# Kernel tuning notes

Hardware: AMD Instinct MI355X
Metric: run time of the kernel (lower is better)

The kernel has to match this reference:

```python
import jax, jax.numpy as jnp
import numpy as np

N = 50000
E = 800000
F_IN = 256
HID = 96
N_CLS = 32
NEG_SLOPE = 0.2


def setup_inputs() -> dict:
    key = jax.random.key(0)
    ks = jax.random.split(key, 10)
    x = jax.random.normal(ks[0], (N, F_IN), dtype=jnp.float32)
    edge_index = jax.random.randint(ks[1], (2, E), 0, N, dtype=jnp.int64)
    s1 = 1.0 / np.sqrt(F_IN)
    s2 = 1.0 / np.sqrt(HID)
    return {
        "x": x,
        "edge_index": edge_index,
        "W1": jax.random.normal(ks[2], (F_IN, HID), dtype=jnp.float32) * s1,
        "a1_src": jax.random.normal(ks[3], (HID,), dtype=jnp.float32) * s2,
        "a1_dst": jax.random.normal(ks[4], (HID,), dtype=jnp.float32) * s2,
        "b1": jnp.zeros((HID,), dtype=jnp.float32),
        "W2": jax.random.normal(ks[5], (HID, N_CLS), dtype=jnp.float32) * s2,
        "a2_src": jax.random.normal(ks[6], (N_CLS,), dtype=jnp.float32) * (1.0 / np.sqrt(N_CLS)),
        "a2_dst": jax.random.normal(ks[7], (N_CLS,), dtype=jnp.float32) * (1.0 / np.sqrt(N_CLS)),
        "b2": jnp.zeros((N_CLS,), dtype=jnp.float32),
    }


def _gat_conv(x, src, dst, W, a_src, a_dst, b, n_nodes):
    # single-head GATConv (PyG defaults), self-loops already in src/dst
    h = x @ W                                  # [N, out]
    alpha_src = h @ a_src                      # [N]
    alpha_dst = h @ a_dst                      # [N]
    e = alpha_src[src] + alpha_dst[dst]        # [E'] edge logits (msg j->i: dst groups)
    e = jnp.where(e > 0, e, NEG_SLOPE * e)     # leaky_relu
    # segment softmax over edges grouped by destination node
    m = jax.ops.segment_max(e, dst, num_segments=n_nodes)
    ex = jnp.exp(e - m[dst])
    denom = jax.ops.segment_sum(ex, dst, num_segments=n_nodes)
    alpha = ex / denom[dst]                    # [E']
    out = jax.ops.segment_sum(alpha[:, None] * h[src], dst, num_segments=n_nodes)
    return out + b


def reference(x, edge_index, W1, a1_src, a1_dst, b1, W2, a2_src, a2_dst, b2):
    loops = jnp.arange(N, dtype=edge_index.dtype)
    src = jnp.concatenate([edge_index[0], loops])
    dst = jnp.concatenate([edge_index[1], loops])
    h = _gat_conv(x, src, dst, W1, a1_src, a1_dst, b1, N)
    h = jax.nn.elu(h)
    # dropout omitted (eval mode, training=False)
    out = _gat_conv(h, src, dst, W2, a2_src, a2_dst, b2, N)
    return jax.nn.log_softmax(out, axis=1)
```

## Files before the change

kernel.cpp:

```cpp
#include <hip/hip_runtime.h>
#include <cstdint>
#include <cstddef>

#define NNODES 50000
#define NEDGES 800000
#define MEDGES (NEDGES + NNODES)
#define FIN    256
#define HID    96
#define NCLS   32
#define NEG_SLOPE 0.2f

#define NBUCK  391
#define BCAP   3072

typedef unsigned int uint32;
typedef __attribute__((ext_vector_type(8))) short short8;
typedef __attribute__((ext_vector_type(4))) float f32x4;

__device__ __forceinline__ ushort bf_round(float f) {
    uint32 u = __float_as_uint(f);
    u += 0x7FFFu + ((u >> 16) & 1u);
    return (ushort)(u >> 16);
}
__device__ __forceinline__ uint32 pack_bf16x2(float a, float b) {
    return (uint32)bf_round(a) | ((uint32)bf_round(b) << 16);
}
__device__ __forceinline__ float bf_lo(uint32 u) { return __uint_as_float(u << 16); }
__device__ __forceinline__ float bf_hi(uint32 u) { return __uint_as_float(u & 0xFFFF0000u); }
__device__ __forceinline__ float lrelu(float t) { return (t > 0.f) ? t : NEG_SLOPE * t; }
__device__ __forceinline__ float af(int i) { return __int_as_float(i); }


__global__ __launch_bounds__(256) void bucket1_kernel(const int* __restrict__ ei,
                                                      int* __restrict__ gcount,
                                                      int* __restrict__ staging) {
    __shared__ int hist[NBUCK];
    __shared__ int base_sh[NBUCK];
    for (int i = threadIdx.x; i < NBUCK; i += 256) hist[i] = 0;
    __syncthreads();

    int v[8], rk[8], bk[8];
    int e0 = blockIdx.x * 2048;
#pragma unroll
    for (int i = 0; i < 8; ++i) {
        int e = e0 + i * 256 + threadIdx.x;
        if (e < MEDGES) {
            int s, d;
            if (e < NEDGES) { s = ei[e]; d = ei[NEDGES + e]; }
            else            { s = e - NEDGES; d = s; }
            bk[i] = d >> 7;
            v[i]  = s | ((d & 127) << 16);
            rk[i] = atomicAdd(&hist[bk[i]], 1);
        } else bk[i] = -1;
    }
    __syncthreads();
    for (int i = threadIdx.x; i < NBUCK; i += 256) {
        int c = hist[i];
        base_sh[i] = c ? atomicAdd(&gcount[i], c) : 0;
    }
    __syncthreads();
#pragma unroll
    for (int i = 0; i < 8; ++i) {
        if (bk[i] >= 0) {
            int pos = base_sh[bk[i]] + rk[i];
            if (pos < BCAP)
                staging[(size_t)bk[i] * BCAP + pos] = v[i];
        }
    }
}

__global__ __launch_bounds__(512) void bscan_kernel(const int* __restrict__ gcount,
                                                    int* __restrict__ bbase) {
    __shared__ int sd[512];
    int t = threadIdx.x;
    int v = (t < NBUCK) ? gcount[t] : 0;
    sd[t] = v;
    __syncthreads();
    for (int off = 1; off < 512; off <<= 1) {
        int val = (t >= off) ? sd[t - off] : 0;
        __syncthreads();
        sd[t] += val;
        __syncthreads();
    }
    if (t < NBUCK) bbase[t] = sd[t] - v;
}

__global__ __launch_bounds__(256) void bucket2_kernel(const int* __restrict__ staging,
                                                      const int* __restrict__ gcount,
                                                      const int* __restrict__ bbase,
                                                      int* __restrict__ rowptr,
                                                      int* __restrict__ esrc) {
    __shared__ int dcount[128];
    __shared__ int dincl[128];
    __shared__ int dexcl[128];
    __shared__ int fillc[128];

    const int b     = blockIdx.x;
    const int t     = threadIdx.x;
    const int cnt   = gcount[b];
    const int ebase = bbase[b];
    const int node0 = b << 7;
    const int* st   = staging + (size_t)b * BCAP;

    for (int i = t; i < 128; i += 256) { dcount[i] = 0; fillc[i] = 0; }
    __syncthreads();

    for (int i = t; i < cnt; i += 256)
        atomicAdd(&dcount[st[i] >> 16], 1);
    __syncthreads();

    if (t < 128) dincl[t] = dcount[t];
    __syncthreads();
    for (int off = 1; off < 128; off <<= 1) {
        int val = (t >= off && t < 128) ? dincl[t - off] : 0;
        __syncthreads();
        if (t < 128) dincl[t] += val;
        __syncthreads();
    }
    if (t < 128) {
        int excl = dincl[t] - dcount[t];
        dexcl[t] = excl;
        int node = node0 + t;
        if (node < NNODES) rowptr[node] = ebase + excl;
    }
    if (b == NBUCK - 1 && t == 0) rowptr[NNODES] = MEDGES;
    __syncthreads();

    for (int i = t; i < cnt; i += 256) {
        int v = st[i];
        int dd = v >> 16;
        int r = atomicAdd(&fillc[dd], 1);
        esrc[ebase + dexcl[dd] + r] = v & 0xFFFF;
    }
}


__global__ __launch_bounds__(256) void packw_kernel(const float* __restrict__ W1,
                                                    const float* __restrict__ W2,
                                                    ushort* __restrict__ W1p,
                                                    ushort* __restrict__ W2p) {
    for (int idx = threadIdx.x; idx < 6 * 8 * 64 * 8; idx += 256) {
        int j     = idx & 7;
        int lane  = (idx >> 3) & 63;
        int kstep = (idx >> 9) & 7;
        int ntile = idx >> 12;
        int k = kstep * 32 + ((lane >> 4) << 3) + j;
        int n = ntile * 16 + (lane & 15);
        W1p[idx] = bf_round(W1[(size_t)k * 96 + n]);
    }
    for (int idx = threadIdx.x; idx < 2 * 3 * 64 * 8; idx += 256) {
        int j     = idx & 7;
        int lane  = (idx >> 3) & 63;
        int kstep = (idx >> 9) % 3;
        int ntile = (idx >> 9) / 3;
        int k = kstep * 32 + ((lane >> 4) << 3) + j;
        int n = ntile * 16 + (lane & 15);
        W2p[idx] = bf_round(W2[(size_t)k * 32 + n]);
    }
}


__global__ __launch_bounds__(256) void gemm1_kernel(const float* __restrict__ x,
                                                    const ushort* __restrict__ W1p,
                                                    const float* __restrict__ a_src,
                                                    const float* __restrict__ a_dst,
                                                    ushort* __restrict__ h1,
                                                    float* __restrict__ as1,
                                                    float* __restrict__ ad1) {
    const int tid  = threadIdx.x;
    const int lane = tid & 63;
    const int wv   = tid >> 6;
    const int m    = lane & 15;
    const int quad = lane >> 4;
    const int node0 = blockIdx.x * 64;

    int arow = node0 + wv * 16 + m;
    if (arow >= NNODES) arow = NNODES - 1;
    const float* xr = x + (size_t)arow * FIN + quad * 8;

    const short8* Wp = (const short8*)W1p;

    f32x4 acc[6];
#pragma unroll
    for (int t = 0; t < 6; ++t) acc[t] = (f32x4){0.f, 0.f, 0.f, 0.f};

#pragma unroll
    for (int ks = 0; ks < 8; ++ks) {
        float4 v0 = *(const float4*)(xr + ks * 32);
        float4 v1 = *(const float4*)(xr + ks * 32 + 4);
        short8 a;
        a[0] = (short)bf_round(v0.x); a[1] = (short)bf_round(v0.y);
        a[2] = (short)bf_round(v0.z); a[3] = (short)bf_round(v0.w);
        a[4] = (short)bf_round(v1.x); a[5] = (short)bf_round(v1.y);
        a[6] = (short)bf_round(v1.z); a[7] = (short)bf_round(v1.w);
#pragma unroll
        for (int t = 0; t < 6; ++t) {
            short8 b = Wp[(t * 8 + ks) * 64 + lane];
            acc[t] = __builtin_amdgcn_mfma_f32_16x16x32_bf16(a, b, acc[t], 0, 0, 0);
        }
    }

    float as_reg[6], ad_reg[6];
#pragma unroll
    for (int t = 0; t < 6; ++t) {
        as_reg[t] = a_src[t * 16 + m];
        ad_reg[t] = a_dst[t * 16 + m];
    }

#pragma unroll
    for (int r = 0; r < 4; ++r) {
        int node = node0 + wv * 16 + quad * 4 + r;
        float ps = 0.f, pd = 0.f;
#pragma unroll
        for (int t = 0; t < 6; ++t) {
            ps += acc[t][r] * as_reg[t];
            pd += acc[t][r] * ad_reg[t];
        }
#pragma unroll
        for (int off = 1; off < 16; off <<= 1) {
            ps += __shfl_xor(ps, off);
            pd += __shfl_xor(pd, off);
        }
        if (node < NNODES) {
            ushort* hp = h1 + (size_t)node * 96 + m;
#pragma unroll
            for (int t = 0; t < 6; ++t) hp[t * 16] = bf_round(acc[t][r]);
            if (m == 0) { as1[node] = ps; ad1[node] = pd; }
        }
    }
}


__global__ __launch_bounds__(256) void gemm2_kernel(const uint32* __restrict__ y48,
                                                    const ushort* __restrict__ W2p,
                                                    const float* __restrict__ a_src,
                                                    const float* __restrict__ a_dst,
                                                    uint32* __restrict__ h2b,
                                                    float* __restrict__ as2,
                                                    float* __restrict__ ad2) {
    const int tid  = threadIdx.x;
    const int lane = tid & 63;
    const int wv   = tid >> 6;
    const int m    = lane & 15;
    const int quad = lane >> 4;
    const int node0 = blockIdx.x * 64;

    int arow = node0 + wv * 16 + m;
    if (arow >= NNODES) arow = NNODES - 1;
    const short8* Ar = (const short8*)(y48 + (size_t)arow * 48);
    const short8* Wp = (const short8*)W2p;

    f32x4 acc[2];
    acc[0] = (f32x4){0.f, 0.f, 0.f, 0.f};
    acc[1] = (f32x4){0.f, 0.f, 0.f, 0.f};

#pragma unroll
    for (int ks = 0; ks < 3; ++ks) {
        short8 a = Ar[ks * 4 + quad];
#pragma unroll
        for (int t = 0; t < 2; ++t) {
            short8 b = Wp[(t * 3 + ks) * 64 + lane];
            acc[t] = __builtin_amdgcn_mfma_f32_16x16x32_bf16(a, b, acc[t], 0, 0, 0);
        }
    }

    float as_reg[2], ad_reg[2];
#pragma unroll
    for (int t = 0; t < 2; ++t) {
        as_reg[t] = a_src[t * 16 + m];
        ad_reg[t] = a_dst[t * 16 + m];
    }

#pragma unroll
    for (int r = 0; r < 4; ++r) {
        int node = node0 + wv * 16 + quad * 4 + r;
        float ps = 0.f, pd = 0.f;
#pragma unroll
        for (int t = 0; t < 2; ++t) {
            ps += acc[t][r] * as_reg[t];
            pd += acc[t][r] * ad_reg[t];
        }
#pragma unroll
        for (int off = 1; off < 16; off <<= 1) {
            ps += __shfl_xor(ps, off);
            pd += __shfl_xor(pd, off);
        }
        if (node < NNODES) {
            h2b[(size_t)node * 16 + m] = pack_bf16x2(acc[0][r], acc[1][r]);
            if (m == 0) { as2[node] = ps; ad2[node] = pd; }
        }
    }
}


__global__ __launch_bounds__(256) void agg96_kernel(const ushort* __restrict__ h,
                                                    const float* __restrict__ asrc,
                                                    const float* __restrict__ adst,
                                                    const float* __restrict__ bias,
                                                    const int* __restrict__ rowptr,
                                                    const int* __restrict__ esrc,
                                                    uint32* __restrict__ out1b) {
    __shared__ int2 sa[4][64];
    int wave = threadIdx.x >> 6;
    int lane = threadIdx.x & 63;
    int i = blockIdx.x * 4 + wave;
    if (i >= NNODES) return;

    int start = rowptr[i], end = rowptr[i + 1];
    int deg = end - start;
    float ad = adst[i];

    if (deg <= 64) {
        int p = start + lane;
        bool valid = p < end;
        int s_reg = valid ? esrc[p] : 0;
        float e = valid ? lrelu(asrc[s_reg] + ad) : -1e30f;
        float mx = e;
#pragma unroll
        for (int off = 32; off; off >>= 1) mx = fmaxf(mx, __shfl_xor(mx, off));
        float ex = valid ? __expf(e - mx) : 0.f;
        float sum = ex;
#pragma unroll
        for (int off = 32; off; off >>= 1) sum += __shfl_xor(sum, off);
        sa[wave][lane] = make_int2(s_reg, __float_as_int(ex / sum));

        const int q   = lane >> 4;
        const int fl  = lane & 15;
        const int flc = (fl < 12) ? fl : 11;
        float acc[8];
#pragma unroll
        for (int j = 0; j < 8; ++j) acc[j] = 0.f;

#pragma unroll 2
        for (int eb = 0; eb < deg; eb += 4) {
            int e0 = eb + q;
            int2 qq = sa[wave][(e0 < 64) ? e0 : 63];
            float a = (fl < 12 && e0 < deg) ? af(qq.y) : 0.f;
            const uint4* hr = (const uint4*)(h + (size_t)qq.x * 96);
            uint4 u = hr[flc];
            acc[0] = fmaf(a, bf_lo(u.x), acc[0]);
            acc[1] = fmaf(a, bf_hi(u.x), acc[1]);
            acc[2] = fmaf(a, bf_lo(u.y), acc[2]);
            acc[3] = fmaf(a, bf_hi(u.y), acc[3]);
            acc[4] = fmaf(a, bf_lo(u.z), acc[4]);
            acc[5] = fmaf(a, bf_hi(u.z), acc[5]);
            acc[6] = fmaf(a, bf_lo(u.w), acc[6]);
            acc[7] = fmaf(a, bf_hi(u.w), acc[7]);
        }
#pragma unroll
        for (int j = 0; j < 8; ++j) {
            acc[j] += __shfl_xor(acc[j], 16);
            acc[j] += __shfl_xor(acc[j], 32);
        }
        if (lane < 12) {
            float v[8];
#pragma unroll
            for (int j = 0; j < 8; ++j) {
                float t = acc[j] + bias[8 * lane + j];
                v[j] = (t > 0.f) ? t : expm1f(t);
            }
            uint4 o;
            o.x = pack_bf16x2(v[0], v[1]);
            o.y = pack_bf16x2(v[2], v[3]);
            o.z = pack_bf16x2(v[4], v[5]);
            o.w = pack_bf16x2(v[6], v[7]);
            *(uint4*)(out1b + (size_t)i * 48 + 4 * lane) = o;
        }
    } else {
        int fl47 = (lane < 48) ? lane : 47;
        float mx = -1e30f;
        for (int p = start + lane; p < end; p += 64)
            mx = fmaxf(mx, lrelu(asrc[esrc[p]] + ad));
#pragma unroll
        for (int off = 32; off; off >>= 1) mx = fmaxf(mx, __shfl_xor(mx, off));
        float sum = 0.f;
        for (int p = start + lane; p < end; p += 64)
            sum += __expf(lrelu(asrc[esrc[p]] + ad) - mx);
#pragma unroll
        for (int off = 32; off; off >>= 1) sum += __shfl_xor(sum, off);
        float inv = 1.f / sum;
        float acc0 = 0.f, acc1 = 0.f;
        for (int p = start; p < end; ++p) {
            int s = esrc[p];
            float a = __expf(lrelu(asrc[s] + ad) - mx) * inv;
            uint32 u = ((const uint32*)(h + (size_t)s * 96))[fl47];
            acc0 += a * bf_lo(u);
            acc1 += a * bf_hi(u);
        }
        if (lane < 48) {
            float v0 = acc0 + bias[2 * lane];
            v0 = (v0 > 0.f) ? v0 : expm1f(v0);
            float v1 = acc1 + bias[2 * lane + 1];
            v1 = (v1 > 0.f) ? v1 : expm1f(v1);
            out1b[(size_t)i * 48 + lane] = pack_bf16x2(v0, v1);
        }
    }
}


__global__ __launch_bounds__(256) void agg32_kernel(const uint32* __restrict__ h2b,
                                                    const float* __restrict__ asrc,
                                                    const float* __restrict__ adst,
                                                    const float* __restrict__ bias,
                                                    const int* __restrict__ rowptr,
                                                    const int* __restrict__ esrc,
                                                    float* __restrict__ out) {
    __shared__ int2 sa[4][64];
    int wave = threadIdx.x >> 6;
    int lane = threadIdx.x & 63;
    int i = blockIdx.x * 4 + wave;
    if (i >= NNODES) return;

    int start = rowptr[i], end = rowptr[i + 1];
    int deg = end - start;
    float ad = adst[i];

    if (deg <= 64) {
        int p = start + lane;
        bool valid = p < end;
        int s_reg = valid ? esrc[p] : 0;
        float e = valid ? lrelu(asrc[s_reg] + ad) : -1e30f;
        float mx = e;
#pragma unroll
        for (int off = 32; off; off >>= 1) mx = fmaxf(mx, __shfl_xor(mx, off));
        float ex = valid ? __expf(e - mx) : 0.f;
        float sum = ex;
#pragma unroll
        for (int off = 32; off; off >>= 1) sum += __shfl_xor(sum, off);
        sa[wave][lane] = make_int2(s_reg, __float_as_int(ex / sum));

        const int g  = lane >> 3;
        const int fl = lane & 7;
        float acc[4];
#pragma unroll
        for (int j = 0; j < 4; ++j) acc[j] = 0.f;

#pragma unroll 2
        for (int eb = 0; eb < deg; eb += 8) {
            int e0 = eb + g;
            int2 qq = sa[wave][(e0 < 64) ? e0 : 63];
            float a = (e0 < deg) ? af(qq.y) : 0.f;
            const uint2* hr = (const uint2*)(h2b + (size_t)qq.x * 16);
            uint2 u = hr[fl];
            acc[0] = fmaf(a, bf_lo(u.x), acc[0]);
            acc[1] = fmaf(a, bf_hi(u.x), acc[1]);
            acc[2] = fmaf(a, bf_lo(u.y), acc[2]);
            acc[3] = fmaf(a, bf_hi(u.y), acc[3]);
        }
#pragma unroll
        for (int j = 0; j < 4; ++j) {
            acc[j] += __shfl_xor(acc[j], 8);
            acc[j] += __shfl_xor(acc[j], 16);
            acc[j] += __shfl_xor(acc[j], 32);
        }

        float z0 = acc[0] + bias[2 * fl];
        float z1 = acc[1] + bias[2 * fl + 16];
        float z2 = acc[2] + bias[2 * fl + 1];
        float z3 = acc[3] + bias[2 * fl + 17];
        float m2 = fmaxf(fmaxf(z0, z1), fmaxf(z2, z3));
#pragma unroll
        for (int off = 4; off; off >>= 1) m2 = fmaxf(m2, __shfl_xor(m2, off));
        float s2 = __expf(z0 - m2) + __expf(z1 - m2) + __expf(z2 - m2) + __expf(z3 - m2);
#pragma unroll
        for (int off = 4; off; off >>= 1) s2 += __shfl_xor(s2, off);
        float ls = m2 + logf(s2);
        if (lane < 8) {
            float* op = out + (size_t)i * 32;
            op[2 * fl]      = z0 - ls;
            op[2 * fl + 16] = z1 - ls;
            op[2 * fl + 1]  = z2 - ls;
            op[2 * fl + 17] = z3 - ls;
        }
    } else {
        int e2 = lane >> 5;
        int f  = lane & 31;
        float mx = -1e30f;
        for (int p = start + lane; p < end; p += 64)
            mx = fmaxf(mx, lrelu(asrc[esrc[p]] + ad));
#pragma unroll
        for (int off = 32; off; off >>= 1) mx = fmaxf(mx, __shfl_xor(mx, off));
        float sum = 0.f;
        for (int p = start + lane; p < end; p += 64)
            sum += __expf(lrelu(asrc[esrc[p]] + ad) - mx);
#pragma unroll
        for (int off = 32; off; off >>= 1) sum += __shfl_xor(sum, off);
        float inv = 1.f / sum;
        float acc = 0.f;
        for (int p = start + e2; p < end; p += 2) {
            int s = esrc[p];
            float a = __expf(lrelu(asrc[s] + ad) - mx) * inv;
            uint32 u = h2b[(size_t)s * 16 + (f & 15)];
            acc += a * ((f < 16) ? bf_lo(u) : bf_hi(u));
        }
        acc += __shfl_xor(acc, 32);

        float z = acc + bias[f];
        float m2 = z;
#pragma unroll
        for (int off = 16; off; off >>= 1) m2 = fmaxf(m2, __shfl_xor(m2, off));
        float ex2 = __expf(z - m2);
        float s2 = ex2;
#pragma unroll
        for (int off = 16; off; off >>= 1) s2 += __shfl_xor(s2, off);
        if (lane < 32) out[(size_t)i * 32 + f] = z - m2 - logf(s2);
    }
}


extern "C" void kernel_launch(void* const* d_in, const int* in_sizes, int n_in,
                              void* d_out, int out_size, void* d_ws, size_t ws_size,
                              hipStream_t stream) {
    const float* x   = (const float*)d_in[0];
    const int*   ei  = (const int*)d_in[1];
    const float* W1  = (const float*)d_in[2];
    const float* a1s = (const float*)d_in[3];
    const float* a1d = (const float*)d_in[4];
    const float* b1  = (const float*)d_in[5];
    const float* W2  = (const float*)d_in[6];
    const float* a2s = (const float*)d_in[7];
    const float* a2d = (const float*)d_in[8];
    const float* b2  = (const float*)d_in[9];
    float* out = (float*)d_out;

    size_t off = 0;
    auto alloc = [&](size_t bytes) {
        void* p = (char*)d_ws + off;
        off += (bytes + 255) & ~(size_t)255;
        return p;
    };
    ushort* h1    = (ushort*)alloc((size_t)NNODES * HID * 2);
    uint32* out1b = (uint32*)alloc((size_t)NNODES * 48 * 4);
    int*  staging = (int*)alloc((size_t)NBUCK * BCAP * 4);
    float* as1    = (float*)alloc((size_t)NNODES * 4);
    float* ad1    = (float*)alloc((size_t)NNODES * 4);
    float* as2    = (float*)alloc((size_t)NNODES * 4);
    float* ad2    = (float*)alloc((size_t)NNODES * 4);
    int*   rowptr = (int*)alloc((size_t)(NNODES + 1) * 4);
    int*   esrc   = (int*)alloc((size_t)MEDGES * 4);
    ushort* W1p   = (ushort*)alloc((size_t)6 * 8 * 64 * 8 * 2);
    ushort* W2p   = (ushort*)alloc((size_t)2 * 3 * 64 * 8 * 2);
    int*   gcount = (int*)alloc((size_t)NBUCK * 4);
    int*   bbase  = (int*)alloc((size_t)NBUCK * 4);
    uint32* h2b   = (uint32*)h1;

    hipMemsetAsync(gcount, 0, (size_t)NBUCK * 4, stream);

    const int nbB1   = (MEDGES + 2047) / 2048;
    const int nbGemm = (NNODES + 63) / 64;
    const int nbAgg  = (NNODES + 3) / 4;

    packw_kernel<<<1, 256, 0, stream>>>(W1, W2, W1p, W2p);
    bucket1_kernel<<<nbB1, 256, 0, stream>>>(ei, gcount, staging);
    bscan_kernel<<<1, 512, 0, stream>>>(gcount, bbase);
    bucket2_kernel<<<NBUCK, 256, 0, stream>>>(staging, gcount, bbase, rowptr, esrc);

    gemm1_kernel<<<nbGemm, 256, 0, stream>>>(x, W1p, a1s, a1d, h1, as1, ad1);
    agg96_kernel<<<nbAgg, 256, 0, stream>>>(h1, as1, ad1, b1, rowptr, esrc, out1b);

    gemm2_kernel<<<nbGemm, 256, 0, stream>>>(out1b, W2p, a2s, a2d, h2b, as2, ad2);
    agg32_kernel<<<nbAgg, 256, 0, stream>>>(h2b, as2, ad2, b2, rowptr, esrc, out);
}
```

Before: 237.5 us.

## Split agg96 into half-waves per node, fold bucket scan, parallelize weight packing

The layer-1 aggregation now assigns one 32-lane half-wave per destination node instead of a full wave. Each lane handles four features, and the low-degree path unrolls eight edge gathers at a time from shared memory to raise memory-level parallelism. The standalone bucket scan kernel is removed: each bucket2 block computes its own base with a block reduction over preceding bucket counts. Weight packing now runs across multiple blocks instead of one. logf and expm1f are replaced with fast intrinsics, which may change accuracy slightly.

```diff
diff --git a/kernel.cpp b/kernel.cpp
--- a/kernel.cpp
+++ b/kernel.cpp
@@ -29,6 +29,7 @@
 __device__ __forceinline__ float bf_hi(uint32 u) { return __uint_as_float(u & 0xFFFF0000u); }
 __device__ __forceinline__ float lrelu(float t) { return (t > 0.f) ? t : NEG_SLOPE * t; }
 __device__ __forceinline__ float af(int i) { return __int_as_float(i); }
+__device__ __forceinline__ float elu_fast(float t) { return (t > 0.f) ? t : (__expf(t) - 1.f); }
 
 
 __global__ __launch_bounds__(256) void bucket1_kernel(const int* __restrict__ ei,
@@ -69,36 +70,29 @@
     }
 }
 
-__global__ __launch_bounds__(512) void bscan_kernel(const int* __restrict__ gcount,
-                                                    int* __restrict__ bbase) {
-    __shared__ int sd[512];
-    int t = threadIdx.x;
-    int v = (t < NBUCK) ? gcount[t] : 0;
-    sd[t] = v;
-    __syncthreads();
-    for (int off = 1; off < 512; off <<= 1) {
-        int val = (t >= off) ? sd[t - off] : 0;
-        __syncthreads();
-        sd[t] += val;
-        __syncthreads();
-    }
-    if (t < NBUCK) bbase[t] = sd[t] - v;
-}
-
 __global__ __launch_bounds__(256) void bucket2_kernel(const int* __restrict__ staging,
                                                       const int* __restrict__ gcount,
-                                                      const int* __restrict__ bbase,
                                                       int* __restrict__ rowptr,
                                                       int* __restrict__ esrc) {
     __shared__ int dcount[128];
     __shared__ int dincl[128];
     __shared__ int dexcl[128];
     __shared__ int fillc[128];
-
-    const int b     = blockIdx.x;
-    const int t     = threadIdx.x;
+    __shared__ int red_s[256];
+
+    const int b = blockIdx.x;
+    const int t = threadIdx.x;
+
+    int pv = 0;
+    for (int idx = t; idx < b; idx += 256) pv += gcount[idx];
+    red_s[t] = pv;
+    __syncthreads();
+    for (int off2 = 128; off2; off2 >>= 1) {
+        if (t < off2) red_s[t] += red_s[t + off2];
+        __syncthreads();
+    }
+    const int ebase = red_s[0];
     const int cnt   = gcount[b];
-    const int ebase = bbase[b];
     const int node0 = b << 7;
     const int* st   = staging + (size_t)b * BCAP;
 
@@ -139,7 +133,8 @@
                                                     const float* __restrict__ W2,
                                                     ushort* __restrict__ W1p,
                                                     ushort* __restrict__ W2p) {
-    for (int idx = threadIdx.x; idx < 6 * 8 * 64 * 8; idx += 256) {
+    int stride = gridDim.x * 256;
+    for (int idx = blockIdx.x * 256 + threadIdx.x; idx < 6 * 8 * 64 * 8; idx += stride) {
         int j     = idx & 7;
         int lane  = (idx >> 3) & 63;
         int kstep = (idx >> 9) & 7;
@@ -148,7 +143,7 @@
         int n = ntile * 16 + (lane & 15);
         W1p[idx] = bf_round(W1[(size_t)k * 96 + n]);
     }
-    for (int idx = threadIdx.x; idx < 2 * 3 * 64 * 8; idx += 256) {
+    for (int idx = blockIdx.x * 256 + threadIdx.x; idx < 2 * 3 * 64 * 8; idx += stride) {
         int j     = idx & 7;
         int lane  = (idx >> 3) & 63;
         int kstep = (idx >> 9) % 3;
@@ -300,100 +295,93 @@
                                                     const int* __restrict__ rowptr,
                                                     const int* __restrict__ esrc,
                                                     uint32* __restrict__ out1b) {
-    __shared__ int2 sa[4][64];
-    int wave = threadIdx.x >> 6;
-    int lane = threadIdx.x & 63;
-    int i = blockIdx.x * 4 + wave;
-    if (i >= NNODES) return;
-
-    int start = rowptr[i], end = rowptr[i + 1];
-    int deg = end - start;
-    float ad = adst[i];
-
-    if (deg <= 64) {
-        int p = start + lane;
-        bool valid = p < end;
-        int s_reg = valid ? esrc[p] : 0;
+    __shared__ int2 sa[4][2][32];
+    const int wave = threadIdx.x >> 6;
+    const int lane = threadIdx.x & 63;
+    const int hf   = lane >> 5;
+    const int fl32 = lane & 31;
+    const int i = blockIdx.x * 8 + wave * 2 + hf;
+
+    const int start = rowptr[i];
+    const int deg   = rowptr[i + 1] - start;
+    const float ad  = adst[i];
+    const int fl    = (fl32 < 24) ? fl32 : 23;
+
+    float acc0 = 0.f, acc1 = 0.f, acc2 = 0.f, acc3 = 0.f;
+
+    if (deg <= 32) {
+        bool valid = fl32 < deg;
+        int s_reg = valid ? esrc[start + fl32] : 0;
         float e = valid ? lrelu(asrc[s_reg] + ad) : -1e30f;
         float mx = e;
 #pragma unroll
-        for (int off = 32; off; off >>= 1) mx = fmaxf(mx, __shfl_xor(mx, off));
+        for (int off = 16; off; off >>= 1) mx = fmaxf(mx, __shfl_xor(mx, off));
         float ex = valid ? __expf(e - mx) : 0.f;
         float sum = ex;
 #pragma unroll
-        for (int off = 32; off; off >>= 1) sum += __shfl_xor(sum, off);
-        sa[wave][lane] = make_int2(s_reg, __float_as_int(ex / sum));
-
-        const int q   = lane >> 4;
-        const int fl  = lane & 15;
-        const int flc = (fl < 12) ? fl : 11;
-        float acc[8];
-#pragma unroll
-        for (int j = 0; j < 8; ++j) acc[j] = 0.f;
-
-#pragma unroll 2
-        for (int eb = 0; eb < deg; eb += 4) {
-            int e0 = eb + q;
-            int2 qq = sa[wave][(e0 < 64) ? e0 : 63];
-            float a = (fl < 12 && e0 < deg) ? af(qq.y) : 0.f;
-            const uint4* hr = (const uint4*)(h + (size_t)qq.x * 96);
-            uint4 u = hr[flc];
-            acc[0] = fmaf(a, bf_lo(u.x), acc[0]);
-            acc[1] = fmaf(a, bf_hi(u.x), acc[1]);
-            acc[2] = fmaf(a, bf_lo(u.y), acc[2]);
-            acc[3] = fmaf(a, bf_hi(u.y), acc[3]);
-            acc[4] = fmaf(a, bf_lo(u.z), acc[4]);
-            acc[5] = fmaf(a, bf_hi(u.z), acc[5]);
-            acc[6] = fmaf(a, bf_lo(u.w), acc[6]);
-            acc[7] = fmaf(a, bf_hi(u.w), acc[7]);
-        }
-#pragma unroll
-        for (int j = 0; j < 8; ++j) {
-            acc[j] += __shfl_xor(acc[j], 16);
-            acc[j] += __shfl_xor(acc[j], 32);
-        }
-        if (lane < 12) {
-            float v[8];
-#pragma unroll
-            for (int j = 0; j < 8; ++j) {
-                float t = acc[j] + bias[8 * lane + j];
-                v[j] = (t > 0.f) ? t : expm1f(t);
-            }
-            uint4 o;
-            o.x = pack_bf16x2(v[0], v[1]);
-            o.y = pack_bf16x2(v[2], v[3]);
-            o.z = pack_bf16x2(v[4], v[5]);
-            o.w = pack_bf16x2(v[6], v[7]);
-            *(uint4*)(out1b + (size_t)i * 48 + 4 * lane) = o;
+        for (int off = 16; off; off >>= 1) sum += __shfl_xor(sum, off);
+        sa[wave][hf][fl32] = make_int2(s_reg, __float_as_int(ex / sum));
+
+        const int4* sap = (const int4*)&sa[wave][hf][0];
+
+        for (int eb = 0; eb < deg; eb += 8) {
+            int4 qa = sap[(eb >> 1) + 0];
+            int4 qb = sap[(eb >> 1) + 1];
+            int4 qc = sap[(eb >> 1) + 2];
+            int4 qd = sap[(eb >> 1) + 3];
+            const uint2* r0 = (const uint2*)(h + (size_t)qa.x * 96);
+            const uint2* r1 = (const uint2*)(h + (size_t)qa.z * 96);
+            const uint2* r2 = (const uint2*)(h + (size_t)qb.x * 96);
+            const uint2* r3 = (const uint2*)(h + (size_t)qb.z * 96);
+            const uint2* r4 = (const uint2*)(h + (size_t)qc.x * 96);
+            const uint2* r5 = (const uint2*)(h + (size_t)qc.z * 96);
+            const uint2* r6 = (const uint2*)(h + (size_t)qd.x * 96);
+            const uint2* r7 = (const uint2*)(h + (size_t)qd.z * 96);
+            uint2 u0 = r0[fl], u1 = r1[fl], u2 = r2[fl], u3 = r3[fl];
+            uint2 u4 = r4[fl], u5 = r5[fl], u6 = r6[fl], u7 = r7[fl];
+            float a0 = af(qa.y), a1 = af(qa.w), a2 = af(qb.y), a3 = af(qb.w);
+            float a4 = af(qc.y), a5 = af(qc.w), a6 = af(qd.y), a7 = af(qd.w);
+            acc0 += a0 * bf_lo(u0.x) + a1 * bf_lo(u1.x) + a2 * bf_lo(u2.x) + a3 * bf_lo(u3.x)
+                  + a4 * bf_lo(u4.x) + a5 * bf_lo(u5.x) + a6 * bf_lo(u6.x) + a7 * bf_lo(u7.x);
+            acc1 += a0 * bf_hi(u0.x) + a1 * bf_hi(u1.x) + a2 * bf_hi(u2.x) + a3 * bf_hi(u3.x)
+                  + a4 * bf_hi(u4.x) + a5 * bf_hi(u5.x) + a6 * bf_hi(u6.x) + a7 * bf_hi(u7.x);
+            acc2 += a0 * bf_lo(u0.y) + a1 * bf_lo(u1.y) + a2 * bf_lo(u2.y) + a3 * bf_lo(u3.y)
+                  + a4 * bf_lo(u4.y) + a5 * bf_lo(u5.y) + a6 * bf_lo(u6.y) + a7 * bf_lo(u7.y);
+            acc3 += a0 * bf_hi(u0.y) + a1 * bf_hi(u1.y) + a2 * bf_hi(u2.y) + a3 * bf_hi(u3.y)
+                  + a4 * bf_hi(u4.y) + a5 * bf_hi(u5.y) + a6 * bf_hi(u6.y) + a7 * bf_hi(u7.y);
         }
     } else {
-        int fl47 = (lane < 48) ? lane : 47;
         float mx = -1e30f;
-        for (int p = start + lane; p < end; p += 64)
+        for (int p = start + fl32; p < start + deg; p += 32)
             mx = fmaxf(mx, lrelu(asrc[esrc[p]] + ad));
 #pragma unroll
-        for (int off = 32; off; off >>= 1) mx = fmaxf(mx, __shfl_xor(mx, off));
+        for (int off = 16; off; off >>= 1) mx = fmaxf(mx, __shfl_xor(mx, off));
         float sum = 0.f;
-        for (int p = start + lane; p < end; p += 64)
+        for (int p = start + fl32; p < start + deg; p += 32)
             sum += __expf(lrelu(asrc[esrc[p]] + ad) - mx);
 #pragma unroll
-        for (int off = 32; off; off >>= 1) sum += __shfl_xor(sum, off);
+        for (int off = 16; off; off >>= 1) sum += __shfl_xor(sum, off);
         float inv = 1.f / sum;
-        float acc0 = 0.f, acc1 = 0.f;
-        for (int p = start; p < end; ++p) {
-            int s = esrc[p];
+        for (int e = 0; e < deg; ++e) {
+            int s = esrc[start + e];
             float a = __expf(lrelu(asrc[s] + ad) - mx) * inv;
-            uint32 u = ((const uint32*)(h + (size_t)s * 96))[fl47];
-            acc0 += a * bf_lo(u);
-            acc1 += a * bf_hi(u);
-        }
-        if (lane < 48) {
-            float v0 = acc0 + bias[2 * lane];
-            v0 = (v0 > 0.f) ? v0 : expm1f(v0);
-            float v1 = acc1 + bias[2 * lane + 1];
-            v1 = (v1 > 0.f) ? v1 : expm1f(v1);
-            out1b[(size_t)i * 48 + lane] = pack_bf16x2(v0, v1);
-        }
+            uint2 u = ((const uint2*)(h + (size_t)s * 96))[fl];
+            acc0 += a * bf_lo(u.x);
+            acc1 += a * bf_hi(u.x);
+            acc2 += a * bf_lo(u.y);
+            acc3 += a * bf_hi(u.y);
+        }
+    }
+
+    if (fl32 < 24) {
+        float v0 = elu_fast(acc0 + bias[4 * fl32 + 0]);
+        float v1 = elu_fast(acc1 + bias[4 * fl32 + 1]);
+        float v2 = elu_fast(acc2 + bias[4 * fl32 + 2]);
+        float v3 = elu_fast(acc3 + bias[4 * fl32 + 3]);
+        uint2 o;
+        o.x = pack_bf16x2(v0, v1);
+        o.y = pack_bf16x2(v2, v3);
+        *(uint2*)(out1b + (size_t)i * 48 + 2 * fl32) = o;
     }
 }
 
@@ -464,7 +452,7 @@
         float s2 = __expf(z0 - m2) + __expf(z1 - m2) + __expf(z2 - m2) + __expf(z3 - m2);
 #pragma unroll
         for (int off = 4; off; off >>= 1) s2 += __shfl_xor(s2, off);
-        float ls = m2 + logf(s2);
+        float ls = m2 + __logf(s2);
         if (lane < 8) {
             float* op = out + (size_t)i * 32;
             op[2 * fl]      = z0 - ls;
@@ -503,7 +491,7 @@
         float s2 = ex2;
 #pragma unroll
         for (int off = 16; off; off >>= 1) s2 += __shfl_xor(s2, off);
-        if (lane < 32) out[(size_t)i * 32 + f] = z - m2 - logf(s2);
+        if (lane < 32) out[(size_t)i * 32 + f] = z - m2 - __logf(s2);
     }
 }
 
@@ -541,23 +529,22 @@
     ushort* W1p   = (ushort*)alloc((size_t)6 * 8 * 64 * 8 * 2);
     ushort* W2p   = (ushort*)alloc((size_t)2 * 3 * 64 * 8 * 2);
     int*   gcount = (int*)alloc((size_t)NBUCK * 4);
-    int*   bbase  = (int*)alloc((size_t)NBUCK * 4);
     uint32* h2b   = (uint32*)h1;
 
     hipMemsetAsync(gcount, 0, (size_t)NBUCK * 4, stream);
 
-    const int nbB1   = (MEDGES + 2047) / 2048;
-    const int nbGemm = (NNODES + 63) / 64;
-    const int nbAgg  = (NNODES + 3) / 4;
-
-    packw_kernel<<<1, 256, 0, stream>>>(W1, W2, W1p, W2p);
+    const int nbB1    = (MEDGES + 2047) / 2048;
+    const int nbGemm  = (NNODES + 63) / 64;
+    const int nbAgg96 = NNODES / 8;
+    const int nbAgg32 = (NNODES + 3) / 4;
+
+    packw_kernel<<<13, 256, 0, stream>>>(W1, W2, W1p, W2p);
     bucket1_kernel<<<nbB1, 256, 0, stream>>>(ei, gcount, staging);
-    bscan_kernel<<<1, 512, 0, stream>>>(gcount, bbase);
-    bucket2_kernel<<<NBUCK, 256, 0, stream>>>(staging, gcount, bbase, rowptr, esrc);
+    bucket2_kernel<<<NBUCK, 256, 0, stream>>>(staging, gcount, rowptr, esrc);
 
     gemm1_kernel<<<nbGemm, 256, 0, stream>>>(x, W1p, a1s, a1d, h1, as1, ad1);
-    agg96_kernel<<<nbAgg, 256, 0, stream>>>(h1, as1, ad1, b1, rowptr, esrc, out1b);
+    agg96_kernel<<<nbAgg96, 256, 0, stream>>>(h1, as1, ad1, b1, rowptr, esrc, out1b);
 
     gemm2_kernel<<<nbGemm, 256, 0, stream>>>(out1b, W2p, a2s, a2d, h2b, as2, ad2);
-    agg32_kernel<<<nbAgg, 256, 0, stream>>>(h2b, as2, ad2, b2, rowptr, esrc, out);
-}
+    agg32_kernel<<<nbAgg32, 256, 0, stream>>>(h2b, as2, ad2, b2, rowptr, esrc, out);
+}
```

Measured after the change: 215.1 us. 1.1x faster.
